# Optimization experiments

Measured on AMD Instinct MI355X. Metric: run time of the kernel, lower is better.

The kernel has to match this reference:

```python
import math
import jax, jax.numpy as jnp
import numpy as np


def kaiser_sinc_filter1d(cutoff, half_width, kernel_size):
    even = kernel_size % 2 == 0
    half_size = kernel_size // 2
    delta_f = 4 * half_width
    A = 2.285 * (half_size - 1) * math.pi * delta_f + 7.95
    if A > 50.0:
        beta = 0.1102 * (A - 8.7)
    elif A >= 21.0:
        beta = 0.5842 * (A - 21) ** 0.4 + 0.07886 * (A - 21.0)
    else:
        beta = 0.0
    window = np.kaiser(kernel_size, beta)  # == torch.kaiser_window(periodic=False)
    if even:
        time = np.arange(-half_size, half_size) + 0.5
    else:
        time = np.arange(kernel_size) - half_size
    if cutoff == 0:
        filt = np.zeros_like(time)
    else:
        filt = 2 * cutoff * window * np.sinc(2 * cutoff * time)
        filt = filt / filt.sum()
    return jnp.asarray(filt, dtype=jnp.float32)  # [K]


def _depthwise_conv1d(x, filt, stride, lhs_dilation, padding):
    # x: [B, C, T]; filt: [K] shared across channels (groups=C depthwise)
    C = x.shape[1]
    K = filt.shape[0]
    w = jnp.broadcast_to(filt.reshape(1, 1, K), (C, 1, K))
    return jax.lax.conv_general_dilated(
        x, w,
        window_strides=(stride,),
        padding=[padding],
        lhs_dilation=(lhs_dilation,),
        dimension_numbers=("NCH", "OIH", "NCH"),
        feature_group_count=C,
    )


UP = 2
DOWN = 2
UP_K = 12
DOWN_K = 12


def setup_inputs() -> dict:
    key = jax.random.key(0)
    B, C, T = 16, 512, 4096
    x = jax.random.normal(key, (B, C, T), dtype=jnp.float32)
    alpha = jnp.zeros((1, C, 1), dtype=jnp.float32)
    beta = jnp.zeros((1, C, 1), dtype=jnp.float32)
    up_filter = kaiser_sinc_filter1d(0.5 / UP, 0.6 / UP, UP_K)
    down_filter = kaiser_sinc_filter1d(0.5 / DOWN, 0.6 / DOWN, DOWN_K)
    return {"x": x, "alpha": alpha, "beta": beta,
            "up_filter": up_filter, "down_filter": down_filter}


def reference(x, alpha, beta, up_filter, down_filter):
    # ---- UpSample1d(ratio=UP, kernel_size=UP_K) ----
    pad = UP_K // UP - 1
    pad_left = pad * UP + (UP_K - UP) // 2
    pad_right = pad * UP + (UP_K - UP + 1) // 2
    xp = jnp.pad(x, ((0, 0), (0, 0), (pad, pad)), mode="edge")  # replicate pad
    # conv_transpose1d(stride=UP) == conv with lhs_dilation=UP, full padding, flipped kernel
    y = UP * _depthwise_conv1d(xp, up_filter[::-1], stride=1,
                               lhs_dilation=UP, padding=(UP_K - 1, UP_K - 1))
    y = y[..., pad_left:-pad_right]  # [B, C, UP*T]

    # ---- SnakeBeta ----
    y = y + 1.0 / (jnp.exp(beta) + 1e-9) * jnp.square(jnp.sin(y * jnp.exp(alpha)))

    # ---- DownSample1d(ratio=DOWN, kernel_size=DOWN_K) via LowPassFilter1d ----
    even = DOWN_K % 2 == 0
    dpl = DOWN_K // 2 - int(even)
    dpr = DOWN_K // 2
    yp = jnp.pad(y, ((0, 0), (0, 0), (dpl, dpr)), mode="edge")
    out = _depthwise_conv1d(yp, down_filter, stride=DOWN,
                            lhs_dilation=1, padding=(0, 0))  # [B, C, T]
    return out
```

## Files before the change

kernel.cpp:

```cpp
#include <hip/hip_runtime.h>
#include <math.h>


#define T_LEN     4096
#define TILE      1024
#define NTHREADS  256
#define BPR       (T_LEN / TILE)
#define XTILE     (TILE + 10)
#define YTILE     (2 * TILE + 10)

__global__ __launch_bounds__(NTHREADS) void aa_act_kernel(
    const float* __restrict__ x,
    const float* __restrict__ alpha,
    const float* __restrict__ beta,
    const float* __restrict__ upf,
    const float* __restrict__ downf,
    float* __restrict__ out,
    int C)
{
    __shared__ float sx[XTILE];
    __shared__ float sy[YTILE];

    const int tid  = threadIdx.x;
    const int blk  = blockIdx.x;
    const int row  = blk >> 2;
    const int o0   = (blk & (BPR - 1)) * TILE;
    const int c    = row % C;

    const float* __restrict__ xr = x + (size_t)row * T_LEN;
    float* __restrict__ outr = out + (size_t)row * T_LEN;

    float u[12], d[12];
#pragma unroll
    for (int i = 0; i < 12; ++i) { u[i] = upf[i]; d[i] = downf[i]; }

    const float ea = __expf(alpha[c]);
    const float rb = 1.0f / (__expf(beta[c]) + 1e-9f);

    for (int i = tid; i < XTILE; i += NTHREADS) {
        int g = o0 - 5 + i;
        g = min(max(g, 0), T_LEN - 1);
        sx[i] = xr[g];
    }
    __syncthreads();

    for (int i = tid; i < YTILE; i += NTHREADS) {
        int t = 2 * o0 - 5 + i;
        t = min(max(t, 0), 2 * T_LEN - 1);
        int s = t >> 1;
        float y;
        if ((t & 1) == 0) {
            int bl = s + 2 - o0;
            y = sx[bl]     * u[11] + sx[bl + 1] * u[9] + sx[bl + 2] * u[7]
              + sx[bl + 3] * u[5]  + sx[bl + 4] * u[3] + sx[bl + 5] * u[1];
        } else {
            int bl = s + 3 - o0;
            y = sx[bl]     * u[10] + sx[bl + 1] * u[8] + sx[bl + 2] * u[6]
              + sx[bl + 3] * u[4]  + sx[bl + 4] * u[2] + sx[bl + 5] * u[0];
        }
        y *= 2.0f;
        float sv = __sinf(y * ea);
        sy[i] = y + rb * sv * sv;
    }
    __syncthreads();

#pragma unroll
    for (int i = 0; i < TILE / NTHREADS; ++i) {
        int lo = i * NTHREADS + tid;
        int base = 2 * lo;
        float acc = 0.0f;
#pragma unroll
        for (int k = 0; k < 12; ++k) acc += sy[base + k] * d[k];
        outr[o0 + lo] = acc;
    }
}

extern "C" void kernel_launch(void* const* d_in, const int* in_sizes, int n_in,
                              void* d_out, int out_size, void* d_ws, size_t ws_size,
                              hipStream_t stream) {
    const float* x     = (const float*)d_in[0];
    const float* alpha = (const float*)d_in[1];
    const float* beta  = (const float*)d_in[2];
    const float* upf   = (const float*)d_in[3];
    const float* downf = (const float*)d_in[4];
    float* out = (float*)d_out;

    const int C    = in_sizes[1];
    const int rows = in_sizes[0] / T_LEN;

    dim3 grid(rows * BPR), block(NTHREADS);
    hipLaunchKernelGGL(aa_act_kernel, grid, block, 0, stream,
                       x, alpha, beta, upf, downf, out, C);
}
```

Baseline: 274.7 us.

## Compute upsample outputs in even/odd pairs and vectorize downsample with float4

The upsample stage now has each thread load six input samples once and produce both the odd and even phase outputs, written as a float2 to shared memory. This removes the per-element parity branch and halves the shared-memory reads. Each thread then computes four consecutive downsampled outputs from registers loaded with float4 reads and stores them as one float4. Edge tiles fix up the clamped boundary samples in a separate pass, which costs an extra barrier and some special-case code.

Measured after the change: 268.2 us. 2.4% less time.

```diff
diff --git a/kernel.cpp b/kernel.cpp
--- a/kernel.cpp
+++ b/kernel.cpp
@@ -4,12 +4,39 @@
 
 #define T_LEN     4096
 #define TILE      1024
-#define NTHREADS  256
+#define NT        256
 #define BPR       (T_LEN / TILE)
-#define XTILE     (TILE + 10)
-#define YTILE     (2 * TILE + 10)
+#define XT        (TILE + 12)
+#define PAIRS     (TILE + 6)
+#define YT        (2 * TILE + 12)
 
-__global__ __launch_bounds__(NTHREADS) void aa_act_kernel(
+__device__ __forceinline__ float yact_gen(const float* sx, int o0, int i,
+                                          float ea, float rb, const float* u) {
+    int t = 2 * o0 - 5 + i;
+    t = min(max(t, 0), 2 * T_LEN - 1);
+    int s = t >> 1;
+    float y = 0.0f;
+    if ((t & 1) == 0) {
+        int gb = s - 3;
+#pragma unroll
+        for (int m = 0; m < 6; ++m) {
+            int g = min(max(gb + m, 0), T_LEN - 1);
+            y = fmaf(sx[g - o0 + 5], u[11 - 2 * m], y);
+        }
+    } else {
+        int gb = s - 2;
+#pragma unroll
+        for (int m = 0; m < 6; ++m) {
+            int g = min(max(gb + m, 0), T_LEN - 1);
+            y = fmaf(sx[g - o0 + 5], u[10 - 2 * m], y);
+        }
+    }
+    y *= 2.0f;
+    float sv = __sinf(y * ea);
+    return fmaf(rb * sv, sv, y);
+}
+
+__global__ __launch_bounds__(NT) void aa_act_kernel(
     const float* __restrict__ x,
     const float* __restrict__ alpha,
     const float* __restrict__ beta,
@@ -18,14 +45,14 @@
     float* __restrict__ out,
     int C)
 {
-    __shared__ float sx[XTILE];
-    __shared__ float sy[YTILE];
+    __shared__ __align__(16) float sx[XT];
+    __shared__ __align__(16) float sy[YT];
 
-    const int tid  = threadIdx.x;
-    const int blk  = blockIdx.x;
-    const int row  = blk >> 2;
-    const int o0   = (blk & (BPR - 1)) * TILE;
-    const int c    = row % C;
+    const int tid = threadIdx.x;
+    const int blk = blockIdx.x;
+    const int row = blk >> 2;
+    const int o0  = (blk & (BPR - 1)) * TILE;
+    const int c   = row % C;
 
     const float* __restrict__ xr = x + (size_t)row * T_LEN;
     float* __restrict__ outr = out + (size_t)row * T_LEN;
@@ -37,42 +64,61 @@
     const float ea = __expf(alpha[c]);
     const float rb = 1.0f / (__expf(beta[c]) + 1e-9f);
 
-    for (int i = tid; i < XTILE; i += NTHREADS) {
-        int g = o0 - 5 + i;
+    for (int j = tid; j < XT; j += NT) {
+        int g = o0 - 5 + j;
         g = min(max(g, 0), T_LEN - 1);
-        sx[i] = xr[g];
+        sx[j] = xr[g];
     }
     __syncthreads();
 
-    for (int i = tid; i < YTILE; i += NTHREADS) {
-        int t = 2 * o0 - 5 + i;
-        t = min(max(t, 0), 2 * T_LEN - 1);
-        int s = t >> 1;
-        float y;
-        if ((t & 1) == 0) {
-            int bl = s + 2 - o0;
-            y = sx[bl]     * u[11] + sx[bl + 1] * u[9] + sx[bl + 2] * u[7]
-              + sx[bl + 3] * u[5]  + sx[bl + 4] * u[3] + sx[bl + 5] * u[1];
-        } else {
-            int bl = s + 3 - o0;
-            y = sx[bl]     * u[10] + sx[bl + 1] * u[8] + sx[bl + 2] * u[6]
-              + sx[bl + 3] * u[4]  + sx[bl + 4] * u[2] + sx[bl + 5] * u[0];
-        }
-        y *= 2.0f;
-        float sv = __sinf(y * ea);
-        sy[i] = y + rb * sv * sv;
+    for (int p = tid; p < PAIRS; p += NT) {
+        float x0 = sx[p],     x1 = sx[p + 1], x2 = sx[p + 2];
+        float x3 = sx[p + 3], x4 = sx[p + 4], x5 = sx[p + 5];
+        float yo = x0 * u[10];
+        yo = fmaf(x1, u[8], yo); yo = fmaf(x2, u[6], yo);
+        yo = fmaf(x3, u[4], yo); yo = fmaf(x4, u[2], yo);
+        yo = fmaf(x5, u[0], yo);
+        float ye = x0 * u[11];
+        ye = fmaf(x1, u[9], ye); ye = fmaf(x2, u[7], ye);
+        ye = fmaf(x3, u[5], ye); ye = fmaf(x4, u[3], ye);
+        ye = fmaf(x5, u[1], ye);
+        yo *= 2.0f; ye *= 2.0f;
+        float so = __sinf(yo * ea);
+        float se = __sinf(ye * ea);
+        float2 pr;
+        pr.x = fmaf(rb * so, so, yo);
+        pr.y = fmaf(rb * se, se, ye);
+        *(float2*)(sy + 2 * p) = pr;
     }
     __syncthreads();
 
+    if (o0 == 0 && tid < 5) {
+        sy[tid] = yact_gen(sx, o0, tid, ea, rb, u);
+    }
+    if (o0 + TILE >= T_LEN && tid < 5) {
+        int i = 2 * TILE + 5 + tid;
+        sy[i] = yact_gen(sx, o0, i, ea, rb, u);
+    }
+    __syncthreads();
+
+    const float4* sy4 = (const float4*)sy;
+    float w[20];
 #pragma unroll
-    for (int i = 0; i < TILE / NTHREADS; ++i) {
-        int lo = i * NTHREADS + tid;
-        int base = 2 * lo;
-        float acc = 0.0f;
+    for (int q = 0; q < 5; ++q) {
+        float4 v = sy4[2 * tid + q];
+        w[4 * q + 0] = v.x; w[4 * q + 1] = v.y;
+        w[4 * q + 2] = v.z; w[4 * q + 3] = v.w;
+    }
+    float a0 = 0.f, a1 = 0.f, a2 = 0.f, a3 = 0.f;
 #pragma unroll
-        for (int k = 0; k < 12; ++k) acc += sy[base + k] * d[k];
-        outr[o0 + lo] = acc;
+    for (int k = 0; k < 12; ++k) {
+        a0 = fmaf(d[k], w[k],     a0);
+        a1 = fmaf(d[k], w[k + 2], a1);
+        a2 = fmaf(d[k], w[k + 4], a2);
+        a3 = fmaf(d[k], w[k + 6], a3);
     }
+    float4 o4; o4.x = a0; o4.y = a1; o4.z = a2; o4.w = a3;
+    ((float4*)(outr + o0))[tid] = o4;
 }
 
 extern "C" void kernel_launch(void* const* d_in, const int* in_sizes, int n_in,
@@ -88,7 +134,7 @@
     const int C    = in_sizes[1];
     const int rows = in_sizes[0] / T_LEN;
 
-    dim3 grid(rows * BPR), block(NTHREADS);
+    dim3 grid(rows * BPR), block(NT);
     hipLaunchKernelGGL(aa_act_kernel, grid, block, 0, stream,
                        x, alpha, beta, upf, downf, out, C);
 }
```

## Vectorize loads and split upsampled signal into even/odd float4 LDS planes

Applied to the files above, without the earlier changes.

Global loads of x now use float4, with the clamped scalar path kept only for edge tiles. Each thread computes four even and four odd upsampled samples from registers and stores them to separate even and odd shared-memory planes. The downsample stage then reads those planes as float4, and each thread writes one float4 of output. This removes the strided scalar LDS traffic and the per-element branching, at the cost of an extra barrier and special fix-up code for replicate padding at the boundaries.

Result: faster. 242.2 us (-11.8%).

```diff
diff --git a/kernel.cpp b/kernel.cpp
--- a/kernel.cpp
+++ b/kernel.cpp
@@ -2,14 +2,15 @@
 #include <math.h>
 
 
-#define T_LEN     4096
-#define TILE      1024
-#define NTHREADS  256
-#define BPR       (T_LEN / TILE)
-#define XTILE     (TILE + 10)
-#define YTILE     (2 * TILE + 10)
+#define T_LEN 4096
+#define TILE  1024
+#define NT    256
+#define BPR   (T_LEN / TILE)
+#define XT4   260
+#define NG    258
+#define PL4   260
 
-__global__ __launch_bounds__(NTHREADS) void aa_act_kernel(
+__global__ __launch_bounds__(NT) void aa_act_kernel(
     const float* __restrict__ x,
     const float* __restrict__ alpha,
     const float* __restrict__ beta,
@@ -18,14 +19,15 @@
     float* __restrict__ out,
     int C)
 {
-    __shared__ float sx[XTILE];
-    __shared__ float sy[YTILE];
+    __shared__ __align__(16) float sx[XT4 * 4];
+    __shared__ __align__(16) float sE[PL4 * 4];
+    __shared__ __align__(16) float sO[PL4 * 4];
 
-    const int tid  = threadIdx.x;
-    const int blk  = blockIdx.x;
-    const int row  = blk >> 2;
-    const int o0   = (blk & (BPR - 1)) * TILE;
-    const int c    = row % C;
+    const int tid = threadIdx.x;
+    const int blk = blockIdx.x;
+    const int row = blk >> 2;
+    const int o0  = (blk & (BPR - 1)) * TILE;
+    const int c   = row % C;
 
     const float* __restrict__ xr = x + (size_t)row * T_LEN;
     float* __restrict__ outr = out + (size_t)row * T_LEN;
@@ -37,42 +39,94 @@
     const float ea = __expf(alpha[c]);
     const float rb = 1.0f / (__expf(beta[c]) + 1e-9f);
 
-    for (int i = tid; i < XTILE; i += NTHREADS) {
-        int g = o0 - 5 + i;
-        g = min(max(g, 0), T_LEN - 1);
-        sx[i] = xr[g];
+    const bool eblk = (o0 == 0) || (o0 + TILE == T_LEN);
+    for (int i4 = tid; i4 < XT4; i4 += NT) {
+        int gi = o0 - 8 + 4 * i4;
+        float4 v;
+        if (!eblk || (unsigned)gi <= (unsigned)(T_LEN - 4)) {
+            v = *(const float4*)(xr + gi);
+        } else {
+            v.x = xr[min(max(gi + 0, 0), T_LEN - 1)];
+            v.y = xr[min(max(gi + 1, 0), T_LEN - 1)];
+            v.z = xr[min(max(gi + 2, 0), T_LEN - 1)];
+            v.w = xr[min(max(gi + 3, 0), T_LEN - 1)];
+        }
+        ((float4*)sx)[i4] = v;
     }
     __syncthreads();
 
-    for (int i = tid; i < YTILE; i += NTHREADS) {
-        int t = 2 * o0 - 5 + i;
-        t = min(max(t, 0), 2 * T_LEN - 1);
-        int s = t >> 1;
-        float y;
-        if ((t & 1) == 0) {
-            int bl = s + 2 - o0;
-            y = sx[bl]     * u[11] + sx[bl + 1] * u[9] + sx[bl + 2] * u[7]
-              + sx[bl + 3] * u[5]  + sx[bl + 4] * u[3] + sx[bl + 5] * u[1];
-        } else {
-            int bl = s + 3 - o0;
-            y = sx[bl]     * u[10] + sx[bl + 1] * u[8] + sx[bl + 2] * u[6]
-              + sx[bl + 3] * u[4]  + sx[bl + 4] * u[2] + sx[bl + 5] * u[0];
+    const float4* sx4 = (const float4*)sx;
+    for (int g = tid; g < NG; g += NT) {
+        float4 A = sx4[g], Bv = sx4[g + 1], Cv = sx4[g + 2];
+        float f[12] = { A.x, A.y, A.z, A.w, Bv.x, Bv.y, Bv.z, Bv.w,
+                        Cv.x, Cv.y, Cv.z, Cv.w };
+        float eo[4], oo[4];
+#pragma unroll
+        for (int r = 0; r < 4; ++r) {
+            float yo = f[r + 3] * u[10];
+            yo = fmaf(f[r + 4], u[8], yo);
+            yo = fmaf(f[r + 5], u[6], yo);
+            yo = fmaf(f[r + 6], u[4], yo);
+            yo = fmaf(f[r + 7], u[2], yo);
+            yo = fmaf(f[r + 8], u[0], yo);
+            float ye = f[r + 3] * u[11];
+            ye = fmaf(f[r + 4], u[9], ye);
+            ye = fmaf(f[r + 5], u[7], ye);
+            ye = fmaf(f[r + 6], u[5], ye);
+            ye = fmaf(f[r + 7], u[3], ye);
+            ye = fmaf(f[r + 8], u[1], ye);
+            yo *= 2.0f; ye *= 2.0f;
+            float so_ = __sinf(yo * ea);
+            float se_ = __sinf(ye * ea);
+            oo[r] = fmaf(rb * so_, so_, yo);
+            eo[r] = fmaf(rb * se_, se_, ye);
         }
-        y *= 2.0f;
-        float sv = __sinf(y * ea);
-        sy[i] = y + rb * sv * sv;
+        float4 ev; ev.x = eo[0]; ev.y = eo[1]; ev.z = eo[2]; ev.w = eo[3];
+        float4 ov; ov.x = oo[0]; ov.y = oo[1]; ov.z = oo[2]; ov.w = oo[3];
+        ((float4*)sE)[g] = ev;
+        ((float4*)sO)[g] = ov;
     }
     __syncthreads();
 
+    if (o0 == 0) {
+        float L = sE[2];
+        if (tid < 2) sE[tid] = L;
+        if (tid < 3) sO[tid] = L;
+    }
+    if (o0 + TILE == T_LEN) {
+        float R = sO[TILE + 2];
+        if (tid < 6) sE[TILE + 2 + tid] = R;
+        if (tid < 5) sO[TILE + 3 + tid] = R;
+    }
+    __syncthreads();
+
+    const float4* e4 = (const float4*)sE;
+    const float4* q4 = (const float4*)sO;
+    float4 E0 = e4[tid], E1 = e4[tid + 1], E2 = e4[tid + 2];
+    float4 O0 = q4[tid], O1 = q4[tid + 1], O2 = q4[tid + 2];
+    float e[12] = { E0.x, E0.y, E0.z, E0.w, E1.x, E1.y, E1.z, E1.w,
+                    E2.x, E2.y, E2.z, E2.w };
+    float o_[12] = { O0.x, O0.y, O0.z, O0.w, O1.x, O1.y, O1.z, O1.w,
+                     O2.x, O2.y, O2.z, O2.w };
+    float acc[4];
 #pragma unroll
-    for (int i = 0; i < TILE / NTHREADS; ++i) {
-        int lo = i * NTHREADS + tid;
-        int base = 2 * lo;
-        float acc = 0.0f;
-#pragma unroll
-        for (int k = 0; k < 12; ++k) acc += sy[base + k] * d[k];
-        outr[o0 + lo] = acc;
+    for (int r = 0; r < 4; ++r) {
+        float a = e[r] * d[1];
+        a = fmaf(e[r + 1], d[3],  a);
+        a = fmaf(e[r + 2], d[5],  a);
+        a = fmaf(e[r + 3], d[7],  a);
+        a = fmaf(e[r + 4], d[9],  a);
+        a = fmaf(e[r + 5], d[11], a);
+        a = fmaf(o_[r],     d[0],  a);
+        a = fmaf(o_[r + 1], d[2],  a);
+        a = fmaf(o_[r + 2], d[4],  a);
+        a = fmaf(o_[r + 3], d[6],  a);
+        a = fmaf(o_[r + 4], d[8],  a);
+        a = fmaf(o_[r + 5], d[10], a);
+        acc[r] = a;
     }
+    float4 o4; o4.x = acc[0]; o4.y = acc[1]; o4.z = acc[2]; o4.w = acc[3];
+    ((float4*)(outr + o0))[tid] = o4;
 }
 
 extern "C" void kernel_launch(void* const* d_in, const int* in_sizes, int n_in,
@@ -88,7 +142,7 @@
     const int C    = in_sizes[1];
     const int rows = in_sizes[0] / T_LEN;
 
-    dim3 grid(rows * BPR), block(NTHREADS);
+    dim3 grid(rows * BPR), block(NT);
     hipLaunchKernelGGL(aa_act_kernel, grid, block, 0, stream,
                        x, alpha, beta, upf, downf, out, C);
 }
```
